# Kernel optimization log

Measured on AMD Instinct MI355X. Metric: run time of the kernel, lower is better.

## Reference

```python
import jax, jax.numpy as jnp
import numpy as np

C = 128
EPS = 1e-5


def _ln(x, g, b):
    m = jnp.mean(x, axis=-1, keepdims=True)
    v = jnp.mean((x - m) ** 2, axis=-1, keepdims=True)
    return (x - m) * jax.lax.rsqrt(v + EPS) * g + b


def setup_inputs() -> dict:
    key = jax.random.key(0)
    ks = jax.random.split(key, 10)
    B, N = 1, 384
    s = 1.0 / np.sqrt(C)
    inp = {
        "z": jax.random.normal(ks[0], (B, N, N, C), dtype=jnp.float32),
        "ln1_g": jnp.ones((C,), jnp.float32),
        "ln1_b": jnp.zeros((C,), jnp.float32),
        "ln2_g": jnp.ones((C,), jnp.float32),
        "ln2_b": jnp.zeros((C,), jnp.float32),
        "Wa": jax.random.uniform(ks[1], (C, C), jnp.float32, -s, s),
        "ba": jnp.zeros((C,), jnp.float32),
        "Wga": jax.random.uniform(ks[2], (C, C), jnp.float32, -s, s),
        "bga": jnp.zeros((C,), jnp.float32),
        "Wb": jax.random.uniform(ks[3], (C, C), jnp.float32, -s, s),
        "bb": jnp.zeros((C,), jnp.float32),
        "Wgb": jax.random.uniform(ks[4], (C, C), jnp.float32, -s, s),
        "bgb": jnp.zeros((C,), jnp.float32),
        "Wg": jax.random.uniform(ks[5], (C, C), jnp.float32, -s, s),
        "bg": jnp.zeros((C,), jnp.float32),
        "Wo": jax.random.uniform(ks[6], (C, C), jnp.float32, -s, s),
        "bo": jnp.zeros((C,), jnp.float32),
    }
    return inp


def reference(z, ln1_g, ln1_b, ln2_g, ln2_b, Wa, ba, Wga, bga, Wb, bb, Wgb, bgb, Wg, bg, Wo, bo):
    # z: (B, i, j, c)
    zn = _ln(z, ln1_g, ln1_b)
    a = (zn @ Wa + ba) * jax.nn.sigmoid(zn @ Wga + bga)      # (B,i,k,c)
    b = (zn @ Wb + bb) * jax.nn.sigmoid(zn @ Wgb + bgb)      # (B,j,k,c)
    gate = jax.nn.sigmoid(zn @ Wg + bg)                      # (B,i,j,c)
    o = jnp.einsum('bikc,bjkc->bijc', a, b)                  # outgoing triangle update
    return gate * (_ln(o, ln2_g, ln2_b) @ Wo + bo)
```

## Files before the change

kernel.cpp:

```cpp
#include <hip/hip_runtime.h>
#include <stdint.h>

typedef _Float16 f16x8 __attribute__((ext_vector_type(8)));
typedef float floatx4 __attribute__((ext_vector_type(4)));

#define RR 147456
#define NC 128
#define NN 384

__device__ inline floatx4 zero4() { floatx4 v; v[0]=0.f; v[1]=0.f; v[2]=0.f; v[3]=0.f; return v; }
__device__ inline float sigmoidf_(float x) { return 1.f / (1.f + __expf(-x)); }

__global__ __launch_bounds__(256) void k0_wt(
    const float* __restrict__ w0, const float* __restrict__ w1,
    const float* __restrict__ w2, const float* __restrict__ w3,
    const float* __restrict__ w4, const float* __restrict__ w5,
    _Float16* __restrict__ wf)
{
  const float* w;
  switch (blockIdx.x) {
    case 0: w = w0; break; case 1: w = w1; break; case 2: w = w2; break;
    case 3: w = w3; break; case 4: w = w4; break; default: w = w5; break;
  }
  _Float16* out = wf + blockIdx.x * 16384;
  const int t = threadIdx.x;
  for (int it = 0; it < 64; ++it) {
    int f = it * 256 + t;
    int j  = f & 7;
    int ln = (f >> 3) & 63;
    int nt = (f >> 9) & 7;
    int k0 = f >> 12;
    int k = k0 * 32 + (ln >> 4) * 8 + j;
    int n = nt * 16 + (ln & 15);
    out[f] = (_Float16)w[k * 128 + n];
  }
}

__global__ __launch_bounds__(256) void k2_ln_gemm(
    const float* __restrict__ z, const float* __restrict__ ln1g, const float* __restrict__ ln1b,
    const _Float16* __restrict__ wf,
    const float* __restrict__ ba, const float* __restrict__ bga,
    const float* __restrict__ bb, const float* __restrict__ bgb,
    const float* __restrict__ bg,
    _Float16* __restrict__ at, _Float16* __restrict__ bt, _Float16* __restrict__ gate)
{
  __shared__ __align__(16) _Float16 zns[64][136];
  const int t = threadIdx.x;
  const int w = t >> 6, lane = t & 63;
  const int l15 = lane & 15, quad = lane >> 4;
  const int r0 = blockIdx.x * 64;
  const int nt0 = w * 2;

  {
    const int g = lane >> 4, h = lane & 15;
    float4 ga = *(const float4*)(ln1g + h*8);
    float4 gb = *(const float4*)(ln1g + h*8 + 4);
    float4 bba = *(const float4*)(ln1b + h*8);
    float4 bbb = *(const float4*)(ln1b + h*8 + 4);
    #pragma unroll
    for (int rr = 0; rr < 4; ++rr) {
      int row = w * 16 + rr * 4 + g;
      const float* zp = z + (size_t)(r0 + row) * NC + h * 8;
      float4 xa = *(const float4*)zp;
      float4 xb = *(const float4*)(zp + 4);
      float s = xa.x + xa.y + xa.z + xa.w + xb.x + xb.y + xb.z + xb.w;
      float q = xa.x*xa.x + xa.y*xa.y + xa.z*xa.z + xa.w*xa.w
              + xb.x*xb.x + xb.y*xb.y + xb.z*xb.z + xb.w*xb.w;
      #pragma unroll
      for (int m = 1; m < 16; m <<= 1) { s += __shfl_xor(s, m); q += __shfl_xor(q, m); }
      float mean = s * (1.f/128.f);
      float var  = q * (1.f/128.f) - mean*mean;
      float rs = rsqrtf(var + 1e-5f);
      union { uint4 u; _Float16 hh[8]; } pk;
      pk.hh[0] = (_Float16)((xa.x - mean) * rs * ga.x + bba.x);
      pk.hh[1] = (_Float16)((xa.y - mean) * rs * ga.y + bba.y);
      pk.hh[2] = (_Float16)((xa.z - mean) * rs * ga.z + bba.z);
      pk.hh[3] = (_Float16)((xa.w - mean) * rs * ga.w + bba.w);
      pk.hh[4] = (_Float16)((xb.x - mean) * rs * gb.x + bbb.x);
      pk.hh[5] = (_Float16)((xb.y - mean) * rs * gb.y + bbb.y);
      pk.hh[6] = (_Float16)((xb.z - mean) * rs * gb.z + bbb.z);
      pk.hh[7] = (_Float16)((xb.w - mean) * rs * gb.w + bbb.w);
      *(uint4*)&zns[row][h * 8] = pk.u;
    }
  }
  __syncthreads();

  f16x8 af[4][4];
  #pragma unroll
  for (int mt = 0; mt < 4; ++mt)
    #pragma unroll
    for (int k0 = 0; k0 < 4; ++k0)
      af[mt][k0] = *(const f16x8*)&zns[mt*16 + l15][k0*32 + quad*8];

  const _Float16* pw = wf + lane * 8;
  auto loadw = [&](f16x8 (&bw)[4][2], int slot) {
    const _Float16* p = pw + slot * 16384;
    #pragma unroll
    for (int k0 = 0; k0 < 4; ++k0)
      #pragma unroll
      for (int j = 0; j < 2; ++j)
        bw[k0][j] = *(const f16x8*)(p + (k0*8 + nt0 + j) * 512);
  };
  auto dogemm = [&](const f16x8 (&bw)[4][2], floatx4 (&acc)[4][2]) {
    #pragma unroll
    for (int mt = 0; mt < 4; ++mt)
      #pragma unroll
      for (int j = 0; j < 2; ++j)
        acc[mt][j] = zero4();
    #pragma unroll
    for (int k0 = 0; k0 < 4; ++k0)
      #pragma unroll
      for (int mt = 0; mt < 4; ++mt) {
        acc[mt][0] = __builtin_amdgcn_mfma_f32_16x16x32_f16(af[mt][k0], bw[k0][0], acc[mt][0], 0, 0, 0);
        acc[mt][1] = __builtin_amdgcn_mfma_f32_16x16x32_f16(af[mt][k0], bw[k0][1], acc[mt][1], 0, 0, 0);
      }
  };
  auto combine_store = [&](const floatx4 (&aP)[4][2], const floatx4 (&aG)[4][2],
                           const float* bia, const float* big, _Float16* dst) {
    #pragma unroll
    for (int j = 0; j < 2; ++j) {
      int c = (nt0 + j)*16 + l15;
      float bav = bia[c], bgv = big[c];
      #pragma unroll
      for (int mt = 0; mt < 4; ++mt) {
        union { uint2 u2; _Float16 h[4]; } pk;
        #pragma unroll
        for (int r = 0; r < 4; ++r) {
          float p  = aP[mt][j][r] + bav;
          float gg = aG[mt][j][r] + bgv;
          pk.h[r] = (_Float16)(p * sigmoidf_(gg));
        }
        *(uint2*)(dst + (size_t)c * RR + r0 + mt*16 + quad*4) = pk.u2;
      }
    }
  };

  f16x8 bwA[4][2], bwB[4][2];
  floatx4 accP[4][2], accG[4][2];

  loadw(bwA, 0);
  loadw(bwB, 1);
  dogemm(bwA, accP);
  loadw(bwA, 2);
  dogemm(bwB, accG);
  combine_store(accP, accG, ba, bga, at);
  loadw(bwB, 3);
  dogemm(bwA, accP);
  loadw(bwA, 4);
  dogemm(bwB, accG);
  combine_store(accP, accG, bb, bgb, bt);
  dogemm(bwA, accG);

  #pragma unroll
  for (int j = 0; j < 2; ++j) {
    int c = (nt0 + j)*16 + l15;
    float bgv = bg[c];
    #pragma unroll
    for (int mt = 0; mt < 4; ++mt) {
      union { uint2 u2; _Float16 h[4]; } pk;
      #pragma unroll
      for (int r = 0; r < 4; ++r)
        pk.h[r] = (_Float16)sigmoidf_(accG[mt][j][r] + bgv);
      *(uint2*)(gate + (size_t)c * RR + r0 + mt*16 + quad*4) = pk.u2;
    }
  }
}

__global__ __launch_bounds__(256) void k3_tri(
    const _Float16* __restrict__ at, const _Float16* __restrict__ bt, float* __restrict__ o)
{
  __shared__ __align__(16) _Float16 As[128][72];
  __shared__ __align__(16) _Float16 Bs[128][72];
  const int t = threadIdx.x;
  const int w = t >> 6, lane = t & 63, l15 = lane & 15, quad = lane >> 4;
  const int c = blockIdx.y;
  const int i0 = (blockIdx.x / 3) * 128, j0 = (blockIdx.x % 3) * 128;
  const int wi = w >> 1, wj = w & 1;
  const size_t base = (size_t)c * RR;
  const _Float16* A  = at + base;
  const _Float16* Bp = bt + base;

  floatx4 acc[4][4];
  #pragma unroll
  for (int mt = 0; mt < 4; ++mt)
    #pragma unroll
    for (int nt = 0; nt < 4; ++nt) acc[mt][nt] = zero4();

  for (int kk = 0; kk < NN; kk += 64) {
    #pragma unroll
    for (int s2 = 0; s2 < 4; ++s2) {
      int f = s2 * 2048 + t * 8;
      int row = f >> 6, k = f & 63;
      *(uint4*)&As[row][k] = *(const uint4*)(A  + (size_t)(i0 + row) * NN + kk + k);
      *(uint4*)&Bs[row][k] = *(const uint4*)(Bp + (size_t)(j0 + row) * NN + kk + k);
    }
    __syncthreads();
    #pragma unroll
    for (int k0 = 0; k0 < 64; k0 += 32) {
      f16x8 af[4], bfr[4];
      #pragma unroll
      for (int mt = 0; mt < 4; ++mt) af[mt]  = *(const f16x8*)&As[wi*64 + mt*16 + l15][k0 + quad*8];
      #pragma unroll
      for (int nt = 0; nt < 4; ++nt) bfr[nt] = *(const f16x8*)&Bs[wj*64 + nt*16 + l15][k0 + quad*8];
      #pragma unroll
      for (int mt = 0; mt < 4; ++mt)
        #pragma unroll
        for (int nt = 0; nt < 4; ++nt)
          acc[mt][nt] = __builtin_amdgcn_mfma_f32_16x16x32_f16(af[mt], bfr[nt], acc[mt][nt], 0, 0, 0);
    }
    __syncthreads();
  }
  #pragma unroll
  for (int mt = 0; mt < 4; ++mt) {
    #pragma unroll
    for (int r = 0; r < 4; ++r) {
      int i = i0 + wi*64 + mt*16 + quad*4 + r;
      float* orow = o + base + (size_t)i * NN + j0 + wj*64;
      #pragma unroll
      for (int nt = 0; nt < 4; ++nt) orow[nt*16 + l15] = acc[mt][nt][r];
    }
  }
}

__global__ __launch_bounds__(256) void k4_out(
    const float* __restrict__ o, const _Float16* __restrict__ gate,
    const float* __restrict__ ln2g, const float* __restrict__ ln2b,
    const _Float16* __restrict__ wo5, const float* __restrict__ bo,
    float* __restrict__ out)
{
  __shared__ __align__(16) float    osb[64][132];
  __shared__ __align__(16) _Float16 ans[64][136];
  const int t = threadIdx.x;
  const int w = t >> 6, lane = t & 63, l15 = lane & 15, quad = lane >> 4;
  const int r0 = blockIdx.x * 64;
  const int nt0 = w * 2;

  #pragma unroll
  for (int it = 0; it < 8; ++it) {
    int f = it * 1024 + t * 4;
    int cx = f >> 6, p = f & 63;
    float4 v = *(const float4*)(o + (size_t)cx * RR + r0 + p);
    osb[p+0][cx] = v.x; osb[p+1][cx] = v.y; osb[p+2][cx] = v.z; osb[p+3][cx] = v.w;
  }
  __syncthreads();

  {
    const int g = lane >> 4, h = lane & 15;
    float4 ga = *(const float4*)(ln2g + h*8);
    float4 gb = *(const float4*)(ln2g + h*8 + 4);
    float4 bba = *(const float4*)(ln2b + h*8);
    float4 bbb = *(const float4*)(ln2b + h*8 + 4);
    #pragma unroll
    for (int rr = 0; rr < 4; ++rr) {
      int row = w * 16 + rr * 4 + g;
      float4 xa = *(const float4*)&osb[row][h*8];
      float4 xb = *(const float4*)&osb[row][h*8 + 4];
      float s = xa.x + xa.y + xa.z + xa.w + xb.x + xb.y + xb.z + xb.w;
      float q = xa.x*xa.x + xa.y*xa.y + xa.z*xa.z + xa.w*xa.w
              + xb.x*xb.x + xb.y*xb.y + xb.z*xb.z + xb.w*xb.w;
      #pragma unroll
      for (int m = 1; m < 16; m <<= 1) { s += __shfl_xor(s, m); q += __shfl_xor(q, m); }
      float mean = s * (1.f/128.f);
      float var  = q * (1.f/128.f) - mean*mean;
      float rs = rsqrtf(var + 1e-5f);
      union { uint4 u; _Float16 hh[8]; } pk;
      pk.hh[0] = (_Float16)((xa.x - mean) * rs * ga.x + bba.x);
      pk.hh[1] = (_Float16)((xa.y - mean) * rs * ga.y + bba.y);
      pk.hh[2] = (_Float16)((xa.z - mean) * rs * ga.z + bba.z);
      pk.hh[3] = (_Float16)((xa.w - mean) * rs * ga.w + bba.w);
      pk.hh[4] = (_Float16)((xb.x - mean) * rs * gb.x + bbb.x);
      pk.hh[5] = (_Float16)((xb.y - mean) * rs * gb.y + bbb.y);
      pk.hh[6] = (_Float16)((xb.z - mean) * rs * gb.z + bbb.z);
      pk.hh[7] = (_Float16)((xb.w - mean) * rs * gb.w + bbb.w);
      *(uint4*)&ans[row][h * 8] = pk.u;
    }
  }
  __syncthreads();

  f16x8 bw[4][2];
  {
    const _Float16* p = wo5 + lane * 8;
    #pragma unroll
    for (int k0 = 0; k0 < 4; ++k0)
      #pragma unroll
      for (int j = 0; j < 2; ++j)
        bw[k0][j] = *(const f16x8*)(p + (k0*8 + nt0 + j) * 512);
  }
  f16x8 af[4][4];
  #pragma unroll
  for (int mt = 0; mt < 4; ++mt)
    #pragma unroll
    for (int k0 = 0; k0 < 4; ++k0)
      af[mt][k0] = *(const f16x8*)&ans[mt*16 + l15][k0*32 + quad*8];

  floatx4 acc[4][2];
  #pragma unroll
  for (int mt = 0; mt < 4; ++mt)
    #pragma unroll
    for (int j = 0; j < 2; ++j) acc[mt][j] = zero4();
  #pragma unroll
  for (int k0 = 0; k0 < 4; ++k0)
    #pragma unroll
    for (int mt = 0; mt < 4; ++mt) {
      acc[mt][0] = __builtin_amdgcn_mfma_f32_16x16x32_f16(af[mt][k0], bw[k0][0], acc[mt][0], 0, 0, 0);
      acc[mt][1] = __builtin_amdgcn_mfma_f32_16x16x32_f16(af[mt][k0], bw[k0][1], acc[mt][1], 0, 0, 0);
    }

  #pragma unroll
  for (int j = 0; j < 2; ++j) {
    int c = (nt0 + j)*16 + l15;
    float bov = bo[c];
    #pragma unroll
    for (int mt = 0; mt < 4; ++mt) {
      union { uint2 u2; _Float16 h[4]; } gk;
      gk.u2 = *(const uint2*)(gate + (size_t)c * RR + r0 + mt*16 + quad*4);
      #pragma unroll
      for (int r = 0; r < 4; ++r) {
        int rl = mt*16 + quad*4 + r;
        out[(size_t)(r0 + rl) * NC + c] = (float)gk.h[r] * (acc[mt][j][r] + bov);
      }
    }
  }
}

extern "C" void kernel_launch(void* const* d_in, const int* in_sizes, int n_in,
                              void* d_out, int out_size, void* d_ws, size_t ws_size,
                              hipStream_t stream) {
  const float* z    = (const float*)d_in[0];
  const float* l1g  = (const float*)d_in[1];
  const float* l1b  = (const float*)d_in[2];
  const float* l2g  = (const float*)d_in[3];
  const float* l2b  = (const float*)d_in[4];
  const float* Wa   = (const float*)d_in[5];
  const float* ba   = (const float*)d_in[6];
  const float* Wga  = (const float*)d_in[7];
  const float* bga  = (const float*)d_in[8];
  const float* Wb   = (const float*)d_in[9];
  const float* bb   = (const float*)d_in[10];
  const float* Wgb  = (const float*)d_in[11];
  const float* bgb  = (const float*)d_in[12];
  const float* Wg   = (const float*)d_in[13];
  const float* bg   = (const float*)d_in[14];
  const float* Wo   = (const float*)d_in[15];
  const float* bo   = (const float*)d_in[16];

  char* ws = (char*)d_ws;
  _Float16* at_  = (_Float16*)(ws + 0);
  _Float16* bt_  = (_Float16*)(ws + 37748736);
  _Float16* gate = (_Float16*)(ws + 75497472);
  float*    o    = (float*)   (ws + 113246208);
  _Float16* wf   = (_Float16*)(ws + 188743680);

  hipLaunchKernelGGL(k0_wt, dim3(6), dim3(256), 0, stream, Wa, Wga, Wb, Wgb, Wg, Wo, wf);
  hipLaunchKernelGGL(k2_ln_gemm, dim3(2304), dim3(256), 0, stream,
                     z, l1g, l1b, wf, ba, bga, bb, bgb, bg, at_, bt_, gate);
  hipLaunchKernelGGL(k3_tri, dim3(9, 128), dim3(256), 0, stream, at_, bt_, o);
  hipLaunchKernelGGL(k4_out, dim3(2304), dim3(256), 0, stream,
                     o, gate, l2g, l2b, wf + 5*16384, bo, (float*)d_out);
}
```

Before: 329.2 us.

## Store triangle output in fp16 and cut register pressure in projection kernels

The triangle kernel now writes its intermediate output as fp16 instead of fp32, which halves the write and read traffic between the triangle and output kernels. The output kernel also drops its separate fp32 staging buffer and reuses one fp16 shared tile. Both GEMM kernels now read A fragments from shared memory inside the MFMA loop instead of holding them all in registers. They keep one weight and accumulator set, storing the gate sigmoid as packed fp16, and declare launch bounds of 4 blocks per CU to raise occupancy. The cost is extra LDS reads and lower precision in the intermediate before the second layernorm.

New measurement: 335.6 us. No clear change (+1.9%).

```diff
diff --git a/kernel.cpp b/kernel.cpp
--- a/kernel.cpp
+++ b/kernel.cpp
@@ -36,7 +36,7 @@
   }
 }
 
-__global__ __launch_bounds__(256) void k2_ln_gemm(
+__global__ __launch_bounds__(256, 4) void k2_ln_gemm(
     const float* __restrict__ z, const float* __restrict__ ln1g, const float* __restrict__ ln1b,
     const _Float16* __restrict__ wf,
     const float* __restrict__ ba, const float* __restrict__ bga,
@@ -85,15 +85,13 @@
   }
   __syncthreads();
 
-  f16x8 af[4][4];
-  #pragma unroll
-  for (int mt = 0; mt < 4; ++mt)
-    #pragma unroll
-    for (int k0 = 0; k0 < 4; ++k0)
-      af[mt][k0] = *(const f16x8*)&zns[mt*16 + l15][k0*32 + quad*8];
-
   const _Float16* pw = wf + lane * 8;
-  auto loadw = [&](f16x8 (&bw)[4][2], int slot) {
+  f16x8 bw[4][2];
+  floatx4 acc[4][2];
+  union PkU { unsigned int u; _Float16 h[2]; };
+  PkU sig[4][2][2];
+
+  auto loadw = [&](int slot) {
     const _Float16* p = pw + slot * 16384;
     #pragma unroll
     for (int k0 = 0; k0 < 4; ++k0)
@@ -101,56 +99,57 @@
       for (int j = 0; j < 2; ++j)
         bw[k0][j] = *(const f16x8*)(p + (k0*8 + nt0 + j) * 512);
   };
-  auto dogemm = [&](const f16x8 (&bw)[4][2], floatx4 (&acc)[4][2]) {
-    #pragma unroll
-    for (int mt = 0; mt < 4; ++mt)
-      #pragma unroll
-      for (int j = 0; j < 2; ++j)
-        acc[mt][j] = zero4();
-    #pragma unroll
-    for (int k0 = 0; k0 < 4; ++k0)
+  auto dogemm = [&]() {
+    #pragma unroll
+    for (int mt = 0; mt < 4; ++mt) {
+      acc[mt][0] = zero4(); acc[mt][1] = zero4();
+      #pragma unroll
+      for (int k0 = 0; k0 < 4; ++k0) {
+        f16x8 af = *(const f16x8*)&zns[mt*16 + l15][k0*32 + quad*8];
+        acc[mt][0] = __builtin_amdgcn_mfma_f32_16x16x32_f16(af, bw[k0][0], acc[mt][0], 0, 0, 0);
+        acc[mt][1] = __builtin_amdgcn_mfma_f32_16x16x32_f16(af, bw[k0][1], acc[mt][1], 0, 0, 0);
+      }
+    }
+  };
+  auto sigpack = [&](const float* big) {
+    #pragma unroll
+    for (int j = 0; j < 2; ++j) {
+      float bgv = big[(nt0 + j)*16 + l15];
       #pragma unroll
       for (int mt = 0; mt < 4; ++mt) {
-        acc[mt][0] = __builtin_amdgcn_mfma_f32_16x16x32_f16(af[mt][k0], bw[k0][0], acc[mt][0], 0, 0, 0);
-        acc[mt][1] = __builtin_amdgcn_mfma_f32_16x16x32_f16(af[mt][k0], bw[k0][1], acc[mt][1], 0, 0, 0);
+        sig[mt][j][0].h[0] = (_Float16)sigmoidf_(acc[mt][j][0] + bgv);
+        sig[mt][j][0].h[1] = (_Float16)sigmoidf_(acc[mt][j][1] + bgv);
+        sig[mt][j][1].h[0] = (_Float16)sigmoidf_(acc[mt][j][2] + bgv);
+        sig[mt][j][1].h[1] = (_Float16)sigmoidf_(acc[mt][j][3] + bgv);
       }
+    }
   };
-  auto combine_store = [&](const floatx4 (&aP)[4][2], const floatx4 (&aG)[4][2],
-                           const float* bia, const float* big, _Float16* dst) {
+  auto combine_store = [&](const float* bia, _Float16* dst) {
     #pragma unroll
     for (int j = 0; j < 2; ++j) {
       int c = (nt0 + j)*16 + l15;
-      float bav = bia[c], bgv = big[c];
+      float bav = bia[c];
       #pragma unroll
       for (int mt = 0; mt < 4; ++mt) {
         union { uint2 u2; _Float16 h[4]; } pk;
-        #pragma unroll
-        for (int r = 0; r < 4; ++r) {
-          float p  = aP[mt][j][r] + bav;
-          float gg = aG[mt][j][r] + bgv;
-          pk.h[r] = (_Float16)(p * sigmoidf_(gg));
-        }
+        pk.h[0] = (_Float16)((acc[mt][j][0] + bav) * (float)sig[mt][j][0].h[0]);
+        pk.h[1] = (_Float16)((acc[mt][j][1] + bav) * (float)sig[mt][j][0].h[1]);
+        pk.h[2] = (_Float16)((acc[mt][j][2] + bav) * (float)sig[mt][j][1].h[0]);
+        pk.h[3] = (_Float16)((acc[mt][j][3] + bav) * (float)sig[mt][j][1].h[1]);
         *(uint2*)(dst + (size_t)c * RR + r0 + mt*16 + quad*4) = pk.u2;
       }
     }
   };
 
-  f16x8 bwA[4][2], bwB[4][2];
-  floatx4 accP[4][2], accG[4][2];
-
-  loadw(bwA, 0);
-  loadw(bwB, 1);
-  dogemm(bwA, accP);
-  loadw(bwA, 2);
-  dogemm(bwB, accG);
-  combine_store(accP, accG, ba, bga, at);
-  loadw(bwB, 3);
-  dogemm(bwA, accP);
-  loadw(bwA, 4);
-  dogemm(bwB, accG);
-  combine_store(accP, accG, bb, bgb, bt);
-  dogemm(bwA, accG);
-
+  loadw(1); dogemm(); sigpack(bga);
+  loadw(0); dogemm();
+  loadw(3);
+  combine_store(ba, at);
+  dogemm(); sigpack(bgb);
+  loadw(2); dogemm();
+  loadw(4);
+  combine_store(bb, bt);
+  dogemm();
   #pragma unroll
   for (int j = 0; j < 2; ++j) {
     int c = (nt0 + j)*16 + l15;
@@ -160,14 +159,14 @@
       union { uint2 u2; _Float16 h[4]; } pk;
       #pragma unroll
       for (int r = 0; r < 4; ++r)
-        pk.h[r] = (_Float16)sigmoidf_(accG[mt][j][r] + bgv);
+        pk.h[r] = (_Float16)sigmoidf_(acc[mt][j][r] + bgv);
       *(uint2*)(gate + (size_t)c * RR + r0 + mt*16 + quad*4) = pk.u2;
     }
   }
 }
 
 __global__ __launch_bounds__(256) void k3_tri(
-    const _Float16* __restrict__ at, const _Float16* __restrict__ bt, float* __restrict__ o)
+    const _Float16* __restrict__ at, const _Float16* __restrict__ bt, _Float16* __restrict__ o)
 {
   __shared__ __align__(16) _Float16 As[128][72];
   __shared__ __align__(16) _Float16 Bs[128][72];
@@ -215,32 +214,32 @@
     #pragma unroll
     for (int r = 0; r < 4; ++r) {
       int i = i0 + wi*64 + mt*16 + quad*4 + r;
-      float* orow = o + base + (size_t)i * NN + j0 + wj*64;
-      #pragma unroll
-      for (int nt = 0; nt < 4; ++nt) orow[nt*16 + l15] = acc[mt][nt][r];
-    }
-  }
-}
-
-__global__ __launch_bounds__(256) void k4_out(
-    const float* __restrict__ o, const _Float16* __restrict__ gate,
+      _Float16* orow = o + base + (size_t)i * NN + j0 + wj*64;
+      #pragma unroll
+      for (int nt = 0; nt < 4; ++nt) orow[nt*16 + l15] = (_Float16)acc[mt][nt][r];
+    }
+  }
+}
+
+__global__ __launch_bounds__(256, 4) void k4_out(
+    const _Float16* __restrict__ o, const _Float16* __restrict__ gate,
     const float* __restrict__ ln2g, const float* __restrict__ ln2b,
     const _Float16* __restrict__ wo5, const float* __restrict__ bo,
     float* __restrict__ out)
 {
-  __shared__ __align__(16) float    osb[64][132];
-  __shared__ __align__(16) _Float16 ans[64][136];
+  __shared__ __align__(16) _Float16 osb[64][136];
   const int t = threadIdx.x;
   const int w = t >> 6, lane = t & 63, l15 = lane & 15, quad = lane >> 4;
   const int r0 = blockIdx.x * 64;
   const int nt0 = w * 2;
 
   #pragma unroll
-  for (int it = 0; it < 8; ++it) {
-    int f = it * 1024 + t * 4;
+  for (int it = 0; it < 4; ++it) {
+    int f = (it * 256 + t) * 8;
     int cx = f >> 6, p = f & 63;
-    float4 v = *(const float4*)(o + (size_t)cx * RR + r0 + p);
-    osb[p+0][cx] = v.x; osb[p+1][cx] = v.y; osb[p+2][cx] = v.z; osb[p+3][cx] = v.w;
+    f16x8 v = *(const f16x8*)(o + (size_t)cx * RR + r0 + p);
+    #pragma unroll
+    for (int i = 0; i < 8; ++i) osb[p + i][cx] = v[i];
   }
   __syncthreads();
 
@@ -253,26 +252,26 @@
     #pragma unroll
     for (int rr = 0; rr < 4; ++rr) {
       int row = w * 16 + rr * 4 + g;
-      float4 xa = *(const float4*)&osb[row][h*8];
-      float4 xb = *(const float4*)&osb[row][h*8 + 4];
-      float s = xa.x + xa.y + xa.z + xa.w + xb.x + xb.y + xb.z + xb.w;
-      float q = xa.x*xa.x + xa.y*xa.y + xa.z*xa.z + xa.w*xa.w
-              + xb.x*xb.x + xb.y*xb.y + xb.z*xb.z + xb.w*xb.w;
+      f16x8 xv = *(const f16x8*)&osb[row][h*8];
+      float x0 = (float)xv[0], x1 = (float)xv[1], x2 = (float)xv[2], x3 = (float)xv[3];
+      float x4 = (float)xv[4], x5 = (float)xv[5], x6 = (float)xv[6], x7 = (float)xv[7];
+      float s = x0+x1+x2+x3+x4+x5+x6+x7;
+      float q = x0*x0+x1*x1+x2*x2+x3*x3+x4*x4+x5*x5+x6*x6+x7*x7;
       #pragma unroll
       for (int m = 1; m < 16; m <<= 1) { s += __shfl_xor(s, m); q += __shfl_xor(q, m); }
       float mean = s * (1.f/128.f);
       float var  = q * (1.f/128.f) - mean*mean;
       float rs = rsqrtf(var + 1e-5f);
       union { uint4 u; _Float16 hh[8]; } pk;
-      pk.hh[0] = (_Float16)((xa.x - mean) * rs * ga.x + bba.x);
-      pk.hh[1] = (_Float16)((xa.y - mean) * rs * ga.y + bba.y);
-      pk.hh[2] = (_Float16)((xa.z - mean) * rs * ga.z + bba.z);
-      pk.hh[3] = (_Float16)((xa.w - mean) * rs * ga.w + bba.w);
-      pk.hh[4] = (_Float16)((xb.x - mean) * rs * gb.x + bbb.x);
-      pk.hh[5] = (_Float16)((xb.y - mean) * rs * gb.y + bbb.y);
-      pk.hh[6] = (_Float16)((xb.z - mean) * rs * gb.z + bbb.z);
-      pk.hh[7] = (_Float16)((xb.w - mean) * rs * gb.w + bbb.w);
-      *(uint4*)&ans[row][h * 8] = pk.u;
+      pk.hh[0] = (_Float16)((x0 - mean) * rs * ga.x + bba.x);
+      pk.hh[1] = (_Float16)((x1 - mean) * rs * ga.y + bba.y);
+      pk.hh[2] = (_Float16)((x2 - mean) * rs * ga.z + bba.z);
+      pk.hh[3] = (_Float16)((x3 - mean) * rs * ga.w + bba.w);
+      pk.hh[4] = (_Float16)((x4 - mean) * rs * gb.x + bbb.x);
+      pk.hh[5] = (_Float16)((x5 - mean) * rs * gb.y + bbb.y);
+      pk.hh[6] = (_Float16)((x6 - mean) * rs * gb.z + bbb.z);
+      pk.hh[7] = (_Float16)((x7 - mean) * rs * gb.w + bbb.w);
+      *(uint4*)&osb[row][h * 8] = pk.u;
     }
   }
   __syncthreads();
@@ -286,25 +285,17 @@
       for (int j = 0; j < 2; ++j)
         bw[k0][j] = *(const f16x8*)(p + (k0*8 + nt0 + j) * 512);
   }
-  f16x8 af[4][4];
-  #pragma unroll
-  for (int mt = 0; mt < 4; ++mt)
-    #pragma unroll
-    for (int k0 = 0; k0 < 4; ++k0)
-      af[mt][k0] = *(const f16x8*)&ans[mt*16 + l15][k0*32 + quad*8];
-
   floatx4 acc[4][2];
   #pragma unroll
-  for (int mt = 0; mt < 4; ++mt)
-    #pragma unroll
-    for (int j = 0; j < 2; ++j) acc[mt][j] = zero4();
-  #pragma unroll
-  for (int k0 = 0; k0 < 4; ++k0)
-    #pragma unroll
-    for (int mt = 0; mt < 4; ++mt) {
-      acc[mt][0] = __builtin_amdgcn_mfma_f32_16x16x32_f16(af[mt][k0], bw[k0][0], acc[mt][0], 0, 0, 0);
-      acc[mt][1] = __builtin_amdgcn_mfma_f32_16x16x32_f16(af[mt][k0], bw[k0][1], acc[mt][1], 0, 0, 0);
-    }
+  for (int mt = 0; mt < 4; ++mt) {
+    acc[mt][0] = zero4(); acc[mt][1] = zero4();
+    #pragma unroll
+    for (int k0 = 0; k0 < 4; ++k0) {
+      f16x8 af = *(const f16x8*)&osb[mt*16 + l15][k0*32 + quad*8];
+      acc[mt][0] = __builtin_amdgcn_mfma_f32_16x16x32_f16(af, bw[k0][0], acc[mt][0], 0, 0, 0);
+      acc[mt][1] = __builtin_amdgcn_mfma_f32_16x16x32_f16(af, bw[k0][1], acc[mt][1], 0, 0, 0);
+    }
+  }
 
   #pragma unroll
   for (int j = 0; j < 2; ++j) {
@@ -348,13 +339,13 @@
   _Float16* at_  = (_Float16*)(ws + 0);
   _Float16* bt_  = (_Float16*)(ws + 37748736);
   _Float16* gate = (_Float16*)(ws + 75497472);
-  float*    o    = (float*)   (ws + 113246208);
+  _Float16* o16  = (_Float16*)(ws + 113246208);
   _Float16* wf   = (_Float16*)(ws + 188743680);
 
   hipLaunchKernelGGL(k0_wt, dim3(6), dim3(256), 0, stream, Wa, Wga, Wb, Wgb, Wg, Wo, wf);
   hipLaunchKernelGGL(k2_ln_gemm, dim3(2304), dim3(256), 0, stream,
                      z, l1g, l1b, wf, ba, bga, bb, bgb, bg, at_, bt_, gate);
-  hipLaunchKernelGGL(k3_tri, dim3(9, 128), dim3(256), 0, stream, at_, bt_, o);
+  hipLaunchKernelGGL(k3_tri, dim3(9, 128), dim3(256), 0, stream, at_, bt_, o16);
   hipLaunchKernelGGL(k4_out, dim3(2304), dim3(256), 0, stream,
-                     o, gate, l2g, l2b, wf + 5*16384, bo, (float*)d_out);
-}
+                     o16, gate, l2g, l2b, wf + 5*16384, bo, (float*)d_out);
+}
```
